# Kernel optimization log

Measured on AMD Instinct MI355X. Metric: run time of the kernel, lower is better.

The kernel has to match this reference:

```python
import jax, jax.numpy as jnp
import numpy as np

B, D, H, W = 16, 512, 32, 32
K = 2048            # n_codes
BETA = 0.25
DECAY = 0.99
EPS = 1e-5


def _l2norm(x):
    # matches F.normalize(x, dim=-1) with eps=1e-12
    n = jnp.linalg.norm(x, axis=-1, keepdims=True)
    return x / jnp.maximum(n, 1e-12)


def setup_inputs() -> dict:
    key = jax.random.key(0)
    k1, k2, k3, k4 = jax.random.split(key, 4)
    z = jax.random.normal(k1, (B, D, H, W), dtype=jnp.float32)
    embeddings = jax.random.normal(k2, (K, D), dtype=jnp.float32) * (1.0 / K)
    N_buf = jax.random.uniform(k3, (K,), dtype=jnp.float32) + 0.5
    z_avg = jax.random.normal(k4, (K, D), dtype=jnp.float32) * (1.0 / K)
    return {"z": z, "embeddings": embeddings, "N_buf": N_buf, "z_avg": z_avg}


def reference(z, embeddings, N_buf, z_avg):
    b, d, h, w = z.shape
    # [B,C,H,W] -> [B,H,W,C] -> [N, D]
    flat = z.transpose(0, 2, 3, 1).reshape(-1, d)          # [N, D]
    z_norm = _l2norm(flat)                                  # [N, D]
    cb_norm = _l2norm(embeddings)                           # [K, D]

    # squared euclidean distances (kept in the same expanded form as source)
    distances = (jnp.sum(z_norm ** 2, axis=1, keepdims=True)
                 + jnp.sum(cb_norm ** 2, axis=1)
                 - 2.0 * jnp.matmul(z_norm, cb_norm.T))     # [N, K]
    distance_prob = jax.nn.softmax(-distances, axis=1)      # [N, K]
    encoding_indices = jnp.argmin(distances, axis=1)        # [N] int

    # NOTE: faithful to source -- gathers rows of z_norm (inputs), not codebook
    emb = z_norm[encoding_indices]                          # [N, D]

    # training-mode EMA statistics (one-hot matmul expressed as segment_sum)
    n_total = jax.ops.segment_sum(jnp.ones_like(encoding_indices, dtype=z.dtype),
                                  encoding_indices, num_segments=K)      # [K]
    encode_sum = jax.ops.segment_sum(z_norm, encoding_indices,
                                     num_segments=K)                     # [K, D]
    N_new = DECAY * N_buf + (1.0 - DECAY) * n_total
    z_avg_new = DECAY * z_avg + (1.0 - DECAY) * encode_sum
    n = jnp.sum(N_new)
    weights = (N_new + EPS) / (n + K * EPS) * n                          # [K]
    embeddings_new = z_avg_new / weights[:, None]                        # [K, D]

    commitment_loss = jnp.mean((z_norm - jax.lax.stop_gradient(emb)) ** 2)
    loss = BETA * commitment_loss
    codebook_sum = jnp.sum(jnp.abs(embeddings_new))

    q = emb.reshape(b, h, w, d).transpose(0, 3, 1, 2)       # [B, D, H, W]
    return (q, distance_prob, commitment_loss, loss, codebook_sum,
            embeddings_new, N_new, z_avg_new)
```

## Files before the change

### kernel.cpp

```cpp
#include <hip/hip_runtime.h>

#define NROW 16384
#define KC   2048
#define DIM  512

typedef __attribute__((ext_vector_type(8))) short  short8;
typedef __attribute__((ext_vector_type(4))) float  floatx4;


__device__ __forceinline__ unsigned short f2bf(float f) {
  unsigned int u = __float_as_uint(f);
  u += 0x7fffu + ((u >> 16) & 1u);
  return (unsigned short)(u >> 16);
}

__global__ void k_cbnorm(const float* __restrict__ emb,
                         unsigned short* __restrict__ cb_bf,
                         float* __restrict__ csq) {
  const int k = blockIdx.x;
  const int t = threadIdx.x;
  const float* row = emb + (size_t)k * DIM;
  float v0 = row[t], v1 = row[t + 256];
  float ss = v0 * v0 + v1 * v1;
#pragma unroll
  for (int o = 32; o; o >>= 1) ss += __shfl_xor(ss, o, 64);
  __shared__ float red[4];
  if ((t & 63) == 0) red[t >> 6] = ss;
  __syncthreads();
  float tot = red[0] + red[1] + red[2] + red[3];
  float r = 1.0f / fmaxf(sqrtf(tot), 1e-12f);
  cb_bf[(size_t)k * DIM + t]       = f2bf(v0 * r);
  cb_bf[(size_t)k * DIM + t + 256] = f2bf(v1 * r);
  if (t == 0) csq[k] = tot * r * r;
}

__global__ void k_transpose(const float* __restrict__ z, float* __restrict__ flatT) {
  __shared__ float tile[32][33];
  const int dt = blockIdx.x;
  const int pt = blockIdx.y;
  const int b  = blockIdx.z;
  const int tx = threadIdx.x & 31;
  const int ty = threadIdx.x >> 5;
  const size_t zb = (size_t)b * (DIM * 1024);
#pragma unroll
  for (int i = 0; i < 4; ++i) {
    int d = dt * 32 + ty + i * 8;
    int p = pt * 32 + tx;
    tile[ty + i * 8][tx] = z[zb + (size_t)d * 1024 + p];
  }
  __syncthreads();
#pragma unroll
  for (int i = 0; i < 4; ++i) {
    int p = pt * 32 + ty + i * 8;
    int d = dt * 32 + tx;
    flatT[(size_t)(b * 1024 + p) * DIM + d] = tile[tx][ty + i * 8];
  }
}

__global__ void k_rownorm(const float* __restrict__ flatT,
                          float* __restrict__ rnorm,
                          unsigned short* __restrict__ zbf) {
  const int n = blockIdx.x;
  const int t = threadIdx.x;
  const float* row = flatT + (size_t)n * DIM;
  float v0 = row[t], v1 = row[t + 256];
  float ss = v0 * v0 + v1 * v1;
#pragma unroll
  for (int o = 32; o; o >>= 1) ss += __shfl_xor(ss, o, 64);
  __shared__ float red[4];
  if ((t & 63) == 0) red[t >> 6] = ss;
  __syncthreads();
  float tot = red[0] + red[1] + red[2] + red[3];
  float r = 1.0f / fmaxf(sqrtf(tot), 1e-12f);
  if (t == 0) rnorm[n] = r;
  zbf[(size_t)n * DIM + t]       = f2bf(v0 * r);
  zbf[(size_t)n * DIM + t + 256] = f2bf(v1 * r);
}

__global__ __launch_bounds__(256) void k_gemm(const unsigned short* __restrict__ A,
                                              const unsigned short* __restrict__ Bm,
                                              float* __restrict__ S) {
  __shared__ alignas(16) unsigned short smA[128 * 64];
  __shared__ alignas(16) unsigned short smB[128 * 64];
  const int tid  = threadIdx.x;
  const int wid  = tid >> 6;
  const int lane = tid & 63;
  const int m0 = blockIdx.x * 128;
  const int n0 = blockIdx.y * 128;
  const int wm = (wid >> 1) * 64;
  const int wn = (wid & 1) * 64;

  floatx4 acc[4][4];
  const floatx4 z4 = {0.f, 0.f, 0.f, 0.f};
#pragma unroll
  for (int mi = 0; mi < 4; ++mi)
#pragma unroll
    for (int ni = 0; ni < 4; ++ni) acc[mi][ni] = z4;

  const int srow_l = tid >> 3;
  const int spb    = tid & 7;

  for (int kt = 0; kt < 8; ++kt) {
    const int kbase = kt * 64;
#pragma unroll
    for (int i = 0; i < 4; ++i) {
      int row = i * 32 + srow_l;
      int lb  = spb ^ (row & 7);
      const short8 va = *(const short8*)(A  + (size_t)(m0 + row) * DIM + kbase + lb * 8);
      const short8 vb = *(const short8*)(Bm + (size_t)(n0 + row) * DIM + kbase + lb * 8);
      *(short8*)&smA[i * 2048 + tid * 8] = va;
      *(short8*)&smB[i * 2048 + tid * 8] = vb;
    }
    __syncthreads();
#pragma unroll
    for (int kk = 0; kk < 2; ++kk) {
      const int q   = lane >> 4;
      const int mr  = lane & 15;
      const int lbq = kk * 4 + q;
      short8 af[4], bfr[4];
#pragma unroll
      for (int mi = 0; mi < 4; ++mi) {
        int row = wm + mi * 16 + mr;
        int pb  = lbq ^ (row & 7);
        af[mi] = *(const short8*)&smA[row * 64 + pb * 8];
      }
#pragma unroll
      for (int ni = 0; ni < 4; ++ni) {
        int row = wn + ni * 16 + mr;
        int pb  = lbq ^ (row & 7);
        bfr[ni] = *(const short8*)&smB[row * 64 + pb * 8];
      }
#pragma unroll
      for (int mi = 0; mi < 4; ++mi)
#pragma unroll
        for (int ni = 0; ni < 4; ++ni)
          acc[mi][ni] = __builtin_amdgcn_mfma_f32_16x16x32_bf16(af[mi], bfr[ni], acc[mi][ni], 0, 0, 0);
    }
    __syncthreads();
  }

  const int col = lane & 15;
  const int rq  = (lane >> 4) * 4;
#pragma unroll
  for (int mi = 0; mi < 4; ++mi)
#pragma unroll
    for (int r = 0; r < 4; ++r) {
      size_t rowoff = (size_t)(m0 + wm + mi * 16 + rq + r) * KC;
#pragma unroll
      for (int ni = 0; ni < 4; ++ni)
        S[rowoff + n0 + wn + ni * 16 + col] = acc[mi][ni][r];
    }
}

#define MARGIN_T 2.0e-2f

__global__ void k_softmax(float* __restrict__ S, const float* __restrict__ csq,
                          int* __restrict__ cand_cnt, int* __restrict__ cand_list) {
  const int n = blockIdx.x;
  const int t = threadIdx.x;
  float* row = S + (size_t)n * KC;
  float tv[8];
  float mx = -3.4e38f;
#pragma unroll
  for (int j = 0; j < 8; ++j) {
    int k = t + j * 256;
    tv[j] = 2.0f * row[k] - csq[k];
    mx = fmaxf(mx, tv[j]);
  }
#pragma unroll
  for (int o = 32; o; o >>= 1) mx = fmaxf(mx, __shfl_xor(mx, o, 64));
  __shared__ float redm[4];
  __shared__ float redsum[4];
  __shared__ int   s_cnt;
  __shared__ int   s_list[16];
  if (t == 0) s_cnt = 0;
  if ((t & 63) == 0) redm[t >> 6] = mx;
  __syncthreads();
  const float MX = fmaxf(fmaxf(redm[0], redm[1]), fmaxf(redm[2], redm[3]));
  float ev[8];
  float sum = 0.f;
#pragma unroll
  for (int j = 0; j < 8; ++j) {
    int k = t + j * 256;
    if (tv[j] >= MX - MARGIN_T) {
      int p = atomicAdd(&s_cnt, 1);
      if (p < 16) s_list[p] = k;
    }
    ev[j] = __expf(tv[j] - MX);
    sum += ev[j];
  }
#pragma unroll
  for (int o = 32; o; o >>= 1) sum += __shfl_xor(sum, o, 64);
  if ((t & 63) == 0) redsum[t >> 6] = sum;
  __syncthreads();
  const float inv = 1.0f / (redsum[0] + redsum[1] + redsum[2] + redsum[3]);
#pragma unroll
  for (int j = 0; j < 8; ++j) row[t + j * 256] = ev[j] * inv;
  if (t < 16 && t < s_cnt) cand_list[n * 16 + t] = s_list[t];
  if (t == 0) cand_cnt[n] = (s_cnt > 16) ? -1 : s_cnt;
}

__global__ void k_fixup(const float* __restrict__ flatT, const float* __restrict__ emb,
                        const int* __restrict__ cand_cnt, const int* __restrict__ cand_list,
                        int* __restrict__ idx) {
  const int n = blockIdx.x;
  const int l = threadIdx.x;
  const int c = cand_cnt[n];
  if (c == 1) {
    if (l == 0) idx[n] = cand_list[n * 16];
    return;
  }
  const float* zr = flatT + (size_t)n * DIM;
  double zs = 0.0;
  for (int d = l; d < DIM; d += 64) { double v = zr[d]; zs += v * v; }
#pragma unroll
  for (int o = 32; o; o >>= 1) zs += __shfl_xor(zs, o, 64);
  double zn = fmax(sqrt(zs), 1e-12);
  double best = 1e300;
  int bestk = 0x7fffffff;
  const int m = (c < 0) ? KC : c;
  for (int ci = 0; ci < m; ++ci) {
    int k = (c < 0) ? ci : cand_list[n * 16 + ci];
    const float* er = emb + (size_t)k * DIM;
    double cs = 0.0, dot = 0.0;
    for (int d = l; d < DIM; d += 64) {
      double e = er[d], zv = zr[d];
      cs += e * e; dot += zv * e;
    }
#pragma unroll
    for (int o = 32; o; o >>= 1) { cs += __shfl_xor(cs, o, 64); dot += __shfl_xor(dot, o, 64); }
    double cn = fmax(sqrt(cs), 1e-12);
    double score = cs / (cn * cn) - 2.0 * dot / (zn * cn);
    if (score < best || (score == best && k < bestk)) { best = score; bestk = k; }
  }
  if (l == 0) idx[n] = bestk;
}

__global__ void k_stats(const float* __restrict__ flatT, const float* __restrict__ rnorm,
                        const int* __restrict__ idx, float* __restrict__ enc_sum,
                        float* __restrict__ n_total, double* __restrict__ cl_part) {
  const int n = blockIdx.x;
  const int t = threadIdx.x;
  const int j = idx[n];
  const float rn = rnorm[n], rj = rnorm[j];
  const float* zr  = flatT + (size_t)n * DIM;
  const float* zjr = flatT + (size_t)j * DIM;
  double cl = 0.0;
#pragma unroll
  for (int i = 0; i < 2; ++i) {
    int d = t + i * 256;
    float zv = zr[d] * rn;
    float evv = zjr[d] * rj;
    float df = zv - evv;
    cl += (double)df * (double)df;
    atomicAdd(&enc_sum[(size_t)j * DIM + d], zv);
  }
#pragma unroll
  for (int o = 32; o; o >>= 1) cl += __shfl_xor(cl, o, 64);
  __shared__ double red[4];
  if ((t & 63) == 0) red[t >> 6] = cl;
  __syncthreads();
  if (t == 0) {
    cl_part[n] = red[0] + red[1] + red[2] + red[3];
    atomicAdd(&n_total[j], 1.0f);
  }
}

__global__ void k_zavg(const float* __restrict__ za, const float* __restrict__ es,
                       float* __restrict__ outz) {
  int i = blockIdx.x * 256 + threadIdx.x;
  outz[i] = 0.99f * za[i] + 0.01f * es[i];
}

__global__ void k_nnew(const float* __restrict__ Nb, const float* __restrict__ nt,
                       float* __restrict__ outN, double* __restrict__ nw) {
  const int t = threadIdx.x;
  double s = 0.0;
#pragma unroll
  for (int i = 0; i < 8; ++i) {
    int k = t + i * 256;
    float v = 0.99f * Nb[k] + 0.01f * nt[k];
    outN[k] = v;
    s += (double)v;
  }
#pragma unroll
  for (int o = 32; o; o >>= 1) s += __shfl_xor(s, o, 64);
  __shared__ double red[4];
  if ((t & 63) == 0) red[t >> 6] = s;
  __syncthreads();
  if (t == 0) nw[0] = red[0] + red[1] + red[2] + red[3];
}

__global__ void k_embnew(const float* __restrict__ zan, const float* __restrict__ Nn,
                         const double* __restrict__ nw, float* __restrict__ oute,
                         double* __restrict__ cbs_part) {
  const int t = threadIdx.x;
  const int i = blockIdx.x * 256 + t;
  const int k = i >> 9;
  const float nv = (float)nw[0];
  const float w = (Nn[k] + 1e-5f) / (nv + 0.02048f) * nv;
  const float e = zan[i] / w;
  oute[i] = e;
  double a = (double)fabsf(e);
#pragma unroll
  for (int o = 32; o; o >>= 1) a += __shfl_xor(a, o, 64);
  __shared__ double red[4];
  if ((t & 63) == 0) red[t >> 6] = a;
  __syncthreads();
  if (t == 0) cbs_part[blockIdx.x] = red[0] + red[1] + red[2] + red[3];
}

__global__ void k_q(const float* __restrict__ flatT, const float* __restrict__ rnorm,
                    const int* __restrict__ idx, float* __restrict__ q) {
  const int o = blockIdx.x * 256 + threadIdx.x;
  const int b = o >> 19;
  const int d = (o >> 10) & 511;
  const int p = o & 1023;
  const int j = idx[(b << 10) + p];
  q[o] = flatT[(size_t)j * DIM + d] * rnorm[j];
}

__global__ void k_final(const double* __restrict__ cl_part, const double* __restrict__ cbs_part,
                        float* __restrict__ out) {
  const int t = threadIdx.x;
  double cl = 0.0, cb = 0.0;
  for (int i = t; i < NROW; i += 256) cl += cl_part[i];
  for (int i = t; i < 4096; i += 256) cb += cbs_part[i];
#pragma unroll
  for (int o = 32; o; o >>= 1) { cl += __shfl_xor(cl, o, 64); cb += __shfl_xor(cb, o, 64); }
  __shared__ double redc[4], redb[4];
  if ((t & 63) == 0) { redc[t >> 6] = cl; redb[t >> 6] = cb; }
  __syncthreads();
  if (t == 0) {
    double clm = (redc[0] + redc[1] + redc[2] + redc[3]) / 8388608.0;
    double cbs = redb[0] + redb[1] + redb[2] + redb[3];
    out[41943040] = (float)clm;
    out[41943041] = (float)(0.25 * clm);
    out[41943042] = (float)cbs;
  }
}

extern "C" void kernel_launch(void* const* d_in, const int* in_sizes, int n_in,
                              void* d_out, int out_size, void* d_ws, size_t ws_size,
                              hipStream_t stream) {
  const float* z   = (const float*)d_in[0];
  const float* emb = (const float*)d_in[1];
  const float* Nb  = (const float*)d_in[2];
  const float* za  = (const float*)d_in[3];
  float* out = (float*)d_out;
  char*  ws  = (char*)d_ws;

  float*          flatT     = (float*)(ws + 0);
  unsigned short* cb_bf     = (unsigned short*)(ws + 33554432);
  float*          csq       = (float*)(ws + 35651584);
  float*          rnorm     = (float*)(ws + 35659776);
  int*            idx       = (int*)(ws + 35725312);
  int*            cand_cnt  = (int*)(ws + 35790848);
  int*            cand_list = (int*)(ws + 35856384);
  double*         cl_part   = (double*)(ws + 36904960);
  double*         cbs_part  = (double*)(ws + 37036032);
  float*          enc_sum   = (float*)(ws + 37068800);
  float*          n_total   = (float*)(ws + 41263104);
  double*         nw        = (double*)(ws + 41271296);

  unsigned short* z_bf  = (unsigned short*)out;
  float* S        = out + 8388608;
  float* out_emb  = out + 41943043;
  float* out_N    = out + 42991619;
  float* out_zav  = out + 42993667;

  hipMemsetAsync(ws + 37068800, 0, 4202496, stream);

  k_cbnorm   <<<KC, 256, 0, stream>>>(emb, cb_bf, csq);
  k_transpose<<<dim3(16, 32, 16), 256, 0, stream>>>(z, flatT);
  k_rownorm  <<<NROW, 256, 0, stream>>>(flatT, rnorm, z_bf);
  k_gemm     <<<dim3(NROW / 128, KC / 128), 256, 0, stream>>>(z_bf, cb_bf, S);
  k_softmax  <<<NROW, 256, 0, stream>>>(S, csq, cand_cnt, cand_list);
  k_fixup    <<<NROW, 64, 0, stream>>>(flatT, emb, cand_cnt, cand_list, idx);
  k_stats    <<<NROW, 256, 0, stream>>>(flatT, rnorm, idx, enc_sum, n_total, cl_part);
  k_zavg     <<<4096, 256, 0, stream>>>(za, enc_sum, out_zav);
  k_nnew     <<<1, 256, 0, stream>>>(Nb, n_total, out_N, nw);
  k_embnew   <<<4096, 256, 0, stream>>>(out_zav, out_N, nw, out_emb, cbs_part);
  k_q        <<<32768, 256, 0, stream>>>(flatT, rnorm, idx, out);
  k_final    <<<1, 256, 0, stream>>>(cl_part, cbs_part, out);
}
```

Measured before the change: 429.1 us.

## Fuse pipeline stages, use direct global-to-LDS loads in GEMM, fold distance epilogue

Row norms are now computed straight from z in a separate strided kernel, so the transpose can write the fp32 rows and the normalized bf16 rows in one pass, which removes the rownorm kernel's reread of flatT. The GEMM stages tiles with global_load_lds instead of register round trips, drops the XOR swizzle, and applies the 2*dot - csq epilogue in place. Softmax, argmin fixup and the EMA statistics are merged into a single per-row kernel, and the z_avg, N and embedding updates are merged into a single per-code kernel. In exchange, removing the swizzle may cause LDS bank conflicts, and every tail block now recomputes the total-N reduction redundantly.

```diff
diff --git a/kernel.cpp b/kernel.cpp
--- a/kernel.cpp
+++ b/kernel.cpp
@@ -13,6 +13,10 @@
   u += 0x7fffu + ((u >> 16) & 1u);
   return (unsigned short)(u >> 16);
 }
+
+#define GLDS(gsrc, ldst) __builtin_amdgcn_global_load_lds( \
+    (const __attribute__((address_space(1))) unsigned int*)(gsrc), \
+    (__attribute__((address_space(3))) unsigned int*)(ldst), 16, 0, 0)
 
 __global__ void k_cbnorm(const float* __restrict__ emb,
                          unsigned short* __restrict__ cb_bf,
@@ -34,13 +38,37 @@
   if (t == 0) csq[k] = tot * r * r;
 }
 
-__global__ void k_transpose(const float* __restrict__ z, float* __restrict__ flatT) {
+__global__ void k_pnorm(const float* __restrict__ z, float* __restrict__ rnorm) {
+  const int b  = blockIdx.x;
+  const int pc = blockIdx.y;
+  const int tx = threadIdx.x & 63;
+  const int ty = threadIdx.x >> 6;
+  const int p  = pc * 64 + tx;
+  const float* zp = z + (size_t)b * (DIM * 1024) + p;
+  float ss = 0.f;
+  for (int d = ty; d < DIM; d += 4) {
+    float v = zp[(size_t)d * 1024];
+    ss += v * v;
+  }
+  __shared__ float red[4][64];
+  red[ty][tx] = ss;
+  __syncthreads();
+  if (ty == 0) {
+    float tot = red[0][tx] + red[1][tx] + red[2][tx] + red[3][tx];
+    rnorm[b * 1024 + p] = 1.0f / fmaxf(sqrtf(tot), 1e-12f);
+  }
+}
+
+__global__ void k_transpose(const float* __restrict__ z, const float* __restrict__ rnorm,
+                            float* __restrict__ flatT, unsigned short* __restrict__ zbf) {
   __shared__ float tile[32][33];
+  __shared__ float srn[32];
   const int dt = blockIdx.x;
   const int pt = blockIdx.y;
   const int b  = blockIdx.z;
   const int tx = threadIdx.x & 31;
   const int ty = threadIdx.x >> 5;
+  if (threadIdx.x < 32) srn[threadIdx.x] = rnorm[b * 1024 + pt * 32 + threadIdx.x];
   const size_t zb = (size_t)b * (DIM * 1024);
 #pragma unroll
   for (int i = 0; i < 4; ++i) {
@@ -53,33 +81,17 @@
   for (int i = 0; i < 4; ++i) {
     int p = pt * 32 + ty + i * 8;
     int d = dt * 32 + tx;
-    flatT[(size_t)(b * 1024 + p) * DIM + d] = tile[tx][ty + i * 8];
-  }
-}
-
-__global__ void k_rownorm(const float* __restrict__ flatT,
-                          float* __restrict__ rnorm,
-                          unsigned short* __restrict__ zbf) {
-  const int n = blockIdx.x;
-  const int t = threadIdx.x;
-  const float* row = flatT + (size_t)n * DIM;
-  float v0 = row[t], v1 = row[t + 256];
-  float ss = v0 * v0 + v1 * v1;
-#pragma unroll
-  for (int o = 32; o; o >>= 1) ss += __shfl_xor(ss, o, 64);
-  __shared__ float red[4];
-  if ((t & 63) == 0) red[t >> 6] = ss;
-  __syncthreads();
-  float tot = red[0] + red[1] + red[2] + red[3];
-  float r = 1.0f / fmaxf(sqrtf(tot), 1e-12f);
-  if (t == 0) rnorm[n] = r;
-  zbf[(size_t)n * DIM + t]       = f2bf(v0 * r);
-  zbf[(size_t)n * DIM + t + 256] = f2bf(v1 * r);
+    float v = tile[tx][ty + i * 8];
+    size_t o = (size_t)(b * 1024 + p) * DIM + d;
+    flatT[o] = v;
+    zbf[o]   = f2bf(v * srn[ty + i * 8]);
+  }
 }
 
 __global__ __launch_bounds__(256) void k_gemm(const unsigned short* __restrict__ A,
                                               const unsigned short* __restrict__ Bm,
-                                              float* __restrict__ S) {
+                                              const float* __restrict__ csq,
+                                              float* __restrict__ T) {
   __shared__ alignas(16) unsigned short smA[128 * 64];
   __shared__ alignas(16) unsigned short smB[128 * 64];
   const int tid  = threadIdx.x;
@@ -97,39 +109,31 @@
 #pragma unroll
     for (int ni = 0; ni < 4; ++ni) acc[mi][ni] = z4;
 
-  const int srow_l = tid >> 3;
-  const int spb    = tid & 7;
+  const int srow = tid >> 3;
+  const int scol = (tid & 7) * 8;
+  const unsigned short* Abase = A  + (size_t)(m0 + srow) * DIM + scol;
+  const unsigned short* Bbase = Bm + (size_t)(n0 + srow) * DIM + scol;
 
   for (int kt = 0; kt < 8; ++kt) {
-    const int kbase = kt * 64;
+    const int kb = kt * 64;
 #pragma unroll
     for (int i = 0; i < 4; ++i) {
-      int row = i * 32 + srow_l;
-      int lb  = spb ^ (row & 7);
-      const short8 va = *(const short8*)(A  + (size_t)(m0 + row) * DIM + kbase + lb * 8);
-      const short8 vb = *(const short8*)(Bm + (size_t)(n0 + row) * DIM + kbase + lb * 8);
-      *(short8*)&smA[i * 2048 + tid * 8] = va;
-      *(short8*)&smB[i * 2048 + tid * 8] = vb;
+      GLDS(Abase + kb + (size_t)i * 32 * DIM, &smA[i * 2048 + tid * 8]);
+      GLDS(Bbase + kb + (size_t)i * 32 * DIM, &smB[i * 2048 + tid * 8]);
     }
     __syncthreads();
+    const int q  = lane >> 4;
+    const int mr = lane & 15;
 #pragma unroll
     for (int kk = 0; kk < 2; ++kk) {
-      const int q   = lane >> 4;
-      const int mr  = lane & 15;
-      const int lbq = kk * 4 + q;
+      const int cb = (kk * 4 + q) * 8;
       short8 af[4], bfr[4];
 #pragma unroll
-      for (int mi = 0; mi < 4; ++mi) {
-        int row = wm + mi * 16 + mr;
-        int pb  = lbq ^ (row & 7);
-        af[mi] = *(const short8*)&smA[row * 64 + pb * 8];
-      }
-#pragma unroll
-      for (int ni = 0; ni < 4; ++ni) {
-        int row = wn + ni * 16 + mr;
-        int pb  = lbq ^ (row & 7);
-        bfr[ni] = *(const short8*)&smB[row * 64 + pb * 8];
-      }
+      for (int mi = 0; mi < 4; ++mi)
+        af[mi] = *(const short8*)&smA[(wm + mi * 16 + mr) * 64 + cb];
+#pragma unroll
+      for (int ni = 0; ni < 4; ++ni)
+        bfr[ni] = *(const short8*)&smB[(wn + ni * 16 + mr) * 64 + cb];
 #pragma unroll
       for (int mi = 0; mi < 4; ++mi)
 #pragma unroll
@@ -141,6 +145,9 @@
 
   const int col = lane & 15;
   const int rq  = (lane >> 4) * 4;
+  float csqv[4];
+#pragma unroll
+  for (int ni = 0; ni < 4; ++ni) csqv[ni] = csq[n0 + wn + ni * 16 + col];
 #pragma unroll
   for (int mi = 0; mi < 4; ++mi)
 #pragma unroll
@@ -148,23 +155,27 @@
       size_t rowoff = (size_t)(m0 + wm + mi * 16 + rq + r) * KC;
 #pragma unroll
       for (int ni = 0; ni < 4; ++ni)
-        S[rowoff + n0 + wn + ni * 16 + col] = acc[mi][ni][r];
+        T[rowoff + n0 + wn + ni * 16 + col] = 2.0f * acc[mi][ni][r] - csqv[ni];
     }
 }
 
 #define MARGIN_T 2.0e-2f
 
-__global__ void k_softmax(float* __restrict__ S, const float* __restrict__ csq,
-                          int* __restrict__ cand_cnt, int* __restrict__ cand_list) {
+__global__ void k_row(float* __restrict__ T, const float* __restrict__ flatT,
+                      const float* __restrict__ emb, const float* __restrict__ rnorm,
+                      int* __restrict__ idx, float* __restrict__ enc_sum,
+                      float* __restrict__ n_total, double* __restrict__ cl_part) {
   const int n = blockIdx.x;
   const int t = threadIdx.x;
-  float* row = S + (size_t)n * KC;
+  const int lane = t & 63;
+  const int wid  = t >> 6;
+  float* row = T + (size_t)n * KC;
+
   float tv[8];
   float mx = -3.4e38f;
 #pragma unroll
   for (int j = 0; j < 8; ++j) {
-    int k = t + j * 256;
-    tv[j] = 2.0f * row[k] - csq[k];
+    tv[j] = row[t + j * 256];
     mx = fmaxf(mx, tv[j]);
   }
 #pragma unroll
@@ -173,8 +184,9 @@
   __shared__ float redsum[4];
   __shared__ int   s_cnt;
   __shared__ int   s_list[16];
+  __shared__ int   s_j;
   if (t == 0) s_cnt = 0;
-  if ((t & 63) == 0) redm[t >> 6] = mx;
+  if (lane == 0) redm[wid] = mx;
   __syncthreads();
   const float MX = fmaxf(fmaxf(redm[0], redm[1]), fmaxf(redm[2], redm[3]));
   float ev[8];
@@ -191,57 +203,45 @@
   }
 #pragma unroll
   for (int o = 32; o; o >>= 1) sum += __shfl_xor(sum, o, 64);
-  if ((t & 63) == 0) redsum[t >> 6] = sum;
+  if (lane == 0) redsum[wid] = sum;
   __syncthreads();
   const float inv = 1.0f / (redsum[0] + redsum[1] + redsum[2] + redsum[3]);
 #pragma unroll
   for (int j = 0; j < 8; ++j) row[t + j * 256] = ev[j] * inv;
-  if (t < 16 && t < s_cnt) cand_list[n * 16 + t] = s_list[t];
-  if (t == 0) cand_cnt[n] = (s_cnt > 16) ? -1 : s_cnt;
-}
-
-__global__ void k_fixup(const float* __restrict__ flatT, const float* __restrict__ emb,
-                        const int* __restrict__ cand_cnt, const int* __restrict__ cand_list,
-                        int* __restrict__ idx) {
-  const int n = blockIdx.x;
-  const int l = threadIdx.x;
-  const int c = cand_cnt[n];
+
+  const int c = s_cnt;
   if (c == 1) {
-    if (l == 0) idx[n] = cand_list[n * 16];
-    return;
-  }
-  const float* zr = flatT + (size_t)n * DIM;
-  double zs = 0.0;
-  for (int d = l; d < DIM; d += 64) { double v = zr[d]; zs += v * v; }
-#pragma unroll
-  for (int o = 32; o; o >>= 1) zs += __shfl_xor(zs, o, 64);
-  double zn = fmax(sqrt(zs), 1e-12);
-  double best = 1e300;
-  int bestk = 0x7fffffff;
-  const int m = (c < 0) ? KC : c;
-  for (int ci = 0; ci < m; ++ci) {
-    int k = (c < 0) ? ci : cand_list[n * 16 + ci];
-    const float* er = emb + (size_t)k * DIM;
-    double cs = 0.0, dot = 0.0;
-    for (int d = l; d < DIM; d += 64) {
-      double e = er[d], zv = zr[d];
-      cs += e * e; dot += zv * e;
-    }
-#pragma unroll
-    for (int o = 32; o; o >>= 1) { cs += __shfl_xor(cs, o, 64); dot += __shfl_xor(dot, o, 64); }
-    double cn = fmax(sqrt(cs), 1e-12);
-    double score = cs / (cn * cn) - 2.0 * dot / (zn * cn);
-    if (score < best || (score == best && k < bestk)) { best = score; bestk = k; }
-  }
-  if (l == 0) idx[n] = bestk;
-}
-
-__global__ void k_stats(const float* __restrict__ flatT, const float* __restrict__ rnorm,
-                        const int* __restrict__ idx, float* __restrict__ enc_sum,
-                        float* __restrict__ n_total, double* __restrict__ cl_part) {
-  const int n = blockIdx.x;
-  const int t = threadIdx.x;
-  const int j = idx[n];
+    if (t == 0) s_j = s_list[0];
+  } else if (wid == 0) {
+    const float* zr = flatT + (size_t)n * DIM;
+    double zs = 0.0;
+    for (int d = lane; d < DIM; d += 64) { double v = zr[d]; zs += v * v; }
+#pragma unroll
+    for (int o = 32; o; o >>= 1) zs += __shfl_xor(zs, o, 64);
+    double zn = fmax(sqrt(zs), 1e-12);
+    double best = 1e300;
+    int bestk = 0x7fffffff;
+    const int m = (c > 16) ? KC : c;
+    for (int ci = 0; ci < m; ++ci) {
+      int k = (c > 16) ? ci : s_list[ci];
+      const float* er = emb + (size_t)k * DIM;
+      double cs = 0.0, dot = 0.0;
+      for (int d = lane; d < DIM; d += 64) {
+        double e = er[d], zv = zr[d];
+        cs += e * e; dot += zv * e;
+      }
+#pragma unroll
+      for (int o = 32; o; o >>= 1) { cs += __shfl_xor(cs, o, 64); dot += __shfl_xor(dot, o, 64); }
+      double cn = fmax(sqrt(cs), 1e-12);
+      double score = cs / (cn * cn) - 2.0 * dot / (zn * cn);
+      if (score < best || (score == best && k < bestk)) { best = score; bestk = k; }
+    }
+    if (lane == 0) s_j = bestk;
+  }
+  __syncthreads();
+  const int j = s_j;
+  if (t == 0) idx[n] = j;
+
   const float rn = rnorm[n], rj = rnorm[j];
   const float* zr  = flatT + (size_t)n * DIM;
   const float* zjr = flatT + (size_t)j * DIM;
@@ -249,65 +249,61 @@
 #pragma unroll
   for (int i = 0; i < 2; ++i) {
     int d = t + i * 256;
-    float zv = zr[d] * rn;
+    float zv  = zr[d] * rn;
     float evv = zjr[d] * rj;
-    float df = zv - evv;
+    float df  = zv - evv;
     cl += (double)df * (double)df;
     atomicAdd(&enc_sum[(size_t)j * DIM + d], zv);
   }
 #pragma unroll
   for (int o = 32; o; o >>= 1) cl += __shfl_xor(cl, o, 64);
-  __shared__ double red[4];
-  if ((t & 63) == 0) red[t >> 6] = cl;
+  __shared__ double redd[4];
+  if (lane == 0) redd[wid] = cl;
   __syncthreads();
   if (t == 0) {
-    cl_part[n] = red[0] + red[1] + red[2] + red[3];
+    cl_part[n] = redd[0] + redd[1] + redd[2] + redd[3];
     atomicAdd(&n_total[j], 1.0f);
   }
 }
 
-__global__ void k_zavg(const float* __restrict__ za, const float* __restrict__ es,
-                       float* __restrict__ outz) {
-  int i = blockIdx.x * 256 + threadIdx.x;
-  outz[i] = 0.99f * za[i] + 0.01f * es[i];
-}
-
-__global__ void k_nnew(const float* __restrict__ Nb, const float* __restrict__ nt,
-                       float* __restrict__ outN, double* __restrict__ nw) {
+__global__ void k_tail(const float* __restrict__ za, const float* __restrict__ es,
+                       const float* __restrict__ Nb, const float* __restrict__ ntot,
+                       float* __restrict__ out_zav, float* __restrict__ outN,
+                       float* __restrict__ out_emb, double* __restrict__ cbs_part) {
+  const int k = blockIdx.x;
   const int t = threadIdx.x;
-  double s = 0.0;
+  const int lane = t & 63, wid = t >> 6;
+  float s = 0.f;
 #pragma unroll
   for (int i = 0; i < 8; ++i) {
-    int k = t + i * 256;
-    float v = 0.99f * Nb[k] + 0.01f * nt[k];
-    outN[k] = v;
-    s += (double)v;
+    int kk = t + i * 256;
+    s += 0.99f * Nb[kk] + 0.01f * ntot[kk];
   }
 #pragma unroll
   for (int o = 32; o; o >>= 1) s += __shfl_xor(s, o, 64);
-  __shared__ double red[4];
-  if ((t & 63) == 0) red[t >> 6] = s;
-  __syncthreads();
-  if (t == 0) nw[0] = red[0] + red[1] + red[2] + red[3];
-}
-
-__global__ void k_embnew(const float* __restrict__ zan, const float* __restrict__ Nn,
-                         const double* __restrict__ nw, float* __restrict__ oute,
-                         double* __restrict__ cbs_part) {
-  const int t = threadIdx.x;
-  const int i = blockIdx.x * 256 + t;
-  const int k = i >> 9;
-  const float nv = (float)nw[0];
-  const float w = (Nn[k] + 1e-5f) / (nv + 0.02048f) * nv;
-  const float e = zan[i] / w;
-  oute[i] = e;
-  double a = (double)fabsf(e);
+  __shared__ float redn[4];
+  if (lane == 0) redn[wid] = s;
+  __syncthreads();
+  const float nv = redn[0] + redn[1] + redn[2] + redn[3];
+  const float Nn = 0.99f * Nb[k] + 0.01f * ntot[k];
+  if (t == 0) outN[k] = Nn;
+  const float w = (Nn + 1e-5f) / (nv + 0.02048f) * nv;
+  double a = 0.0;
+#pragma unroll
+  for (int i = 0; i < 2; ++i) {
+    size_t gi = (size_t)k * DIM + t + i * 256;
+    float zv = 0.99f * za[gi] + 0.01f * es[gi];
+    out_zav[gi] = zv;
+    float e = zv / w;
+    out_emb[gi] = e;
+    a += (double)fabsf(e);
+  }
 #pragma unroll
   for (int o = 32; o; o >>= 1) a += __shfl_xor(a, o, 64);
   __shared__ double red[4];
-  if ((t & 63) == 0) red[t >> 6] = a;
-  __syncthreads();
-  if (t == 0) cbs_part[blockIdx.x] = red[0] + red[1] + red[2] + red[3];
+  if (lane == 0) red[wid] = a;
+  __syncthreads();
+  if (t == 0) cbs_part[k] = red[0] + red[1] + red[2] + red[3];
 }
 
 __global__ void k_q(const float* __restrict__ flatT, const float* __restrict__ rnorm,
@@ -325,7 +321,7 @@
   const int t = threadIdx.x;
   double cl = 0.0, cb = 0.0;
   for (int i = t; i < NROW; i += 256) cl += cl_part[i];
-  for (int i = t; i < 4096; i += 256) cb += cbs_part[i];
+  for (int i = t; i < KC; i += 256) cb += cbs_part[i];
 #pragma unroll
   for (int o = 32; o; o >>= 1) { cl += __shfl_xor(cl, o, 64); cb += __shfl_xor(cb, o, 64); }
   __shared__ double redc[4], redb[4];
@@ -355,13 +351,10 @@
   float*          csq       = (float*)(ws + 35651584);
   float*          rnorm     = (float*)(ws + 35659776);
   int*            idx       = (int*)(ws + 35725312);
-  int*            cand_cnt  = (int*)(ws + 35790848);
-  int*            cand_list = (int*)(ws + 35856384);
-  double*         cl_part   = (double*)(ws + 36904960);
-  double*         cbs_part  = (double*)(ws + 37036032);
-  float*          enc_sum   = (float*)(ws + 37068800);
-  float*          n_total   = (float*)(ws + 41263104);
-  double*         nw        = (double*)(ws + 41271296);
+  double*         cl_part   = (double*)(ws + 35790848);
+  double*         cbs_part  = (double*)(ws + 35921920);
+  float*          enc_sum   = (float*)(ws + 35938304);
+  float*          n_total   = (float*)(ws + 40132608);
 
   unsigned short* z_bf  = (unsigned short*)out;
   float* S        = out + 8388608;
@@ -369,18 +362,14 @@
   float* out_N    = out + 42991619;
   float* out_zav  = out + 42993667;
 
-  hipMemsetAsync(ws + 37068800, 0, 4202496, stream);
+  hipMemsetAsync(ws + 35938304, 0, 4202496, stream);
 
   k_cbnorm   <<<KC, 256, 0, stream>>>(emb, cb_bf, csq);
-  k_transpose<<<dim3(16, 32, 16), 256, 0, stream>>>(z, flatT);
-  k_rownorm  <<<NROW, 256, 0, stream>>>(flatT, rnorm, z_bf);
-  k_gemm     <<<dim3(NROW / 128, KC / 128), 256, 0, stream>>>(z_bf, cb_bf, S);
-  k_softmax  <<<NROW, 256, 0, stream>>>(S, csq, cand_cnt, cand_list);
-  k_fixup    <<<NROW, 64, 0, stream>>>(flatT, emb, cand_cnt, cand_list, idx);
-  k_stats    <<<NROW, 256, 0, stream>>>(flatT, rnorm, idx, enc_sum, n_total, cl_part);
-  k_zavg     <<<4096, 256, 0, stream>>>(za, enc_sum, out_zav);
-  k_nnew     <<<1, 256, 0, stream>>>(Nb, n_total, out_N, nw);
-  k_embnew   <<<4096, 256, 0, stream>>>(out_zav, out_N, nw, out_emb, cbs_part);
+  k_pnorm    <<<dim3(16, 16), 256, 0, stream>>>(z, rnorm);
+  k_transpose<<<dim3(16, 32, 16), 256, 0, stream>>>(z, rnorm, flatT, z_bf);
+  k_gemm     <<<dim3(NROW / 128, KC / 128), 256, 0, stream>>>(z_bf, cb_bf, csq, S);
+  k_row      <<<NROW, 256, 0, stream>>>(S, flatT, emb, rnorm, idx, enc_sum, n_total, cl_part);
+  k_tail     <<<KC, 256, 0, stream>>>(za, enc_sum, Nb, n_total, out_zav, out_N, out_emb, cbs_part);
   k_q        <<<32768, 256, 0, stream>>>(flatT, rnorm, idx, out);
   k_final    <<<1, 256, 0, stream>>>(cl_part, cbs_part, out);
 }
```

Result: slower. 468.1 us (+9.1%).
